# Kernel optimization log

Hardware: AMD Instinct MI355X
Metric: run time of the kernel (lower is better)

Reference implementation:

```python
import jax, jax.numpy as jnp
import numpy as np

# Geometry constants (match init_kwargs)
PHI, T, H, W = 720, 512, 256, 256
ANGLE_RATIO = 1.0
RHO = float(np.sqrt(2.0))          # radius of detector span: ||max_pt-min_pt||/2 for [-1,1]^2
DPHI = float(np.pi) * ANGLE_RATIO / PHI   # uniform angle cell width (== mean angle step)
DT = 2.0 * RHO / T                 # detector cell width
T0 = -RHO + 0.5 * DT               # first detector cell center
DX = 2.0 / H                       # pixel width


def setup_inputs() -> dict:
    key = jax.random.key(0)
    k1, k2 = jax.random.split(key)
    sinos = jax.random.normal(k1, (32, PHI, T), dtype=jnp.float32)
    kernel = jax.random.normal(k2, (T // 2 + 1,), dtype=jnp.float32)
    return {"sinos": sinos, "kernel": kernel}


def _backproject(sino):
    """Parallel-beam backprojection (adjoint Radon), linear interp in t.

    sino: [B, PHI, T] -> image [B, H, W].
    f(x) = sum_phi g(phi, x.cos(phi)+y.sin(phi)) * dphi, zero outside detector.
    """
    angles = (jnp.arange(PHI, dtype=sino.dtype) + 0.5) * DPHI  # cell centers
    xs = (-1.0 + (jnp.arange(H, dtype=sino.dtype) + 0.5) * DX)
    X, Y = jnp.meshgrid(xs, xs, indexing='ij')  # [H, W] pixel centers

    def step(acc, inp):
        g, ang = inp                         # g: [B, T] sinogram slice at angle ang
        t = X * jnp.cos(ang) + Y * jnp.sin(ang)   # [H, W] detector coordinate
        u = (t - T0) / DT                    # fractional detector index
        i0 = jnp.floor(u)
        w = u - i0
        i0 = i0.astype(jnp.int32)
        i1 = i0 + 1
        w0 = jnp.where((i0 >= 0) & (i0 < T), 1.0 - w, 0.0)
        w1 = jnp.where((i1 >= 0) & (i1 < T), w, 0.0)
        i0c = jnp.clip(i0, 0, T - 1)
        i1c = jnp.clip(i1, 0, T - 1)
        v = g[:, i0c] * w0 + g[:, i1c] * w1  # [B, H, W]
        return acc + v, None

    B = sino.shape[0]
    acc0 = jnp.zeros((B, H, W), dtype=sino.dtype)
    sino_p = jnp.moveaxis(sino, 1, 0)        # [PHI, B, T] for scan over angles
    acc, _ = jax.lax.scan(step, acc0, (sino_p, angles))
    return acc * DPHI


def reference(sinos, kernel):
    # FFT-domain 1D filtering along detector axis, then backprojection
    filtered = jnp.fft.irfft(jnp.fft.rfft(sinos, axis=-1) * kernel, n=T, axis=-1)
    return _backproject(filtered.astype(sinos.dtype))
```

## Files before the change

kernel.cpp:

```cpp
#include <hip/hip_runtime.h>
#include <hip/hip_bf16.h>

#define NPHI 720
#define NT   512
#define NH   256
#define NB   32

#define DPHI_F   0.004363323129985824f
#define INV_DT_F 181.01933598375618f
#define DX_F     0.0078125f
#define W2PI_F   0.012271846303085130f

#define FSTR 520

typedef __fp16  h2   __attribute__((ext_vector_type(2)));
typedef _Float16 f16x2 __attribute__((ext_vector_type(2)));
typedef _Float16 f16x8 __attribute__((ext_vector_type(8)));
typedef float    f32x4 __attribute__((ext_vector_type(4)));
typedef float    f32x4u __attribute__((ext_vector_type(4), aligned(4)));
typedef float    f32x2u __attribute__((ext_vector_type(2), aligned(4)));

__device__ __forceinline__ float fdot2f(h2 a, float b_bits, float c) {
    return __builtin_amdgcn_fdot2(__builtin_bit_cast(f16x2, a),
                                  __builtin_bit_cast(f16x2, b_bits), c, false);
}

__global__ __launch_bounds__(256) void setup_kernel(const float* __restrict__ kern,
                                                    float* __restrict__ ws,
                                                    unsigned int* __restrict__ Ht,
                                                    float4* __restrict__ out4,
                                                    float* __restrict__ filt) {
    const int bid = (int)blockIdx.x;
    const int tid = threadIdx.x;
    if (bid < 64) {
        __shared__ float ctab[512];
        __shared__ float kk[257];
        __shared__ float hloc[512];
        kk[tid] = kern[tid];
        if (tid == 0) kk[256] = kern[256];
        ctab[tid]       = cosf((float)tid * W2PI_F);
        ctab[tid + 256] = cosf((float)(tid + 256) * W2PI_F);
        __syncthreads();
        for (int tt = tid; tt < 512; tt += 256) {
            float acc = 0.f;
            for (int k = 1; k < 256; ++k)
                acc += kk[k] * ctab[(k * tt) & 511];
            hloc[tt] = (kk[0] + ((tt & 1) ? -kk[256] : kk[256]) + 2.f * acc) * (1.f / 512.f);
        }
        __syncthreads();
        const int o  = bid * 8 + (tid >> 5);
        const int c0 = tid & 31;
        unsigned int* dst = Ht + (size_t)o * 256;
        #pragma unroll
        for (int k = 0; k < 8; ++k) {
            int mp = c0 + 32 * k;
            h2 p = __builtin_amdgcn_cvt_pkrtz(hloc[(o - 2 * mp) & 511],
                                              hloc[(o - 2 * mp - 1) & 511]);
            dst[mp] = __builtin_bit_cast(unsigned int, p);
        }
    } else if (bid < 67) {
        int p = (bid - 64) * 256 + tid;
        if (p < NPHI) {
            float ang = ((float)p + 0.5f) * DPHI_F;
            float s, c;
            sincosf(ang, &s, &c);
            float cd = c * INV_DT_F;
            float sd = s * INV_DT_F;
            ws[512 + 4 * p + 0] = cd;
            ws[512 + 4 * p + 1] = sd;
            ws[512 + 4 * p + 2] = cd * DX_F;
            ws[512 + 4 * p + 3] = sd * DX_F;
        }
    } else if (bid < 195) {
        const float4 z = make_float4(0.f, 0.f, 0.f, 0.f);
        const int nout4 = NB * NH * NH / 4;
        for (int i = (bid - 67) * 256 + tid; i < nout4; i += 128 * 256)
            out4[i] = z;
    } else {
        const float4 z = make_float4(0.f, 0.f, 0.f, 0.f);
        const int rb = (bid - 195) * 180;
        for (int i = tid; i < 360; i += 256) {
            int row = rb + (i >> 1);
            float* p = filt + (size_t)row * FSTR + ((i & 1) ? 516 : 0);
            *(float4*)p = z;
        }
    }
}

#define ASTR 40
#define BSTR 40

__global__ __launch_bounds__(512) void conv_gemm_kernel(const float* __restrict__ g,
                                                        const unsigned short* __restrict__ Ht,
                                                        float* __restrict__ filt) {
    __shared__ __attribute__((aligned(16))) unsigned short As[64 * ASTR];
    __shared__ __attribute__((aligned(16))) unsigned short Bs[512 * BSTR];
    const int tid = threadIdx.x;
    const int m0 = (int)blockIdx.x * 64;

    const int w = tid >> 6, l = tid & 63;
    const int wm = (w >> 2) * 32;
    const int wn = (w & 3) * 128;
    const int fr = l & 15, g16 = l >> 4;

    const int arow = tid >> 3, aq = (tid & 7) * 4;

    f32x4 acc[2][8];
    #pragma unroll
    for (int i = 0; i < 2; ++i)
        #pragma unroll
        for (int j = 0; j < 8; ++j) acc[i][j] = (f32x4){0.f, 0.f, 0.f, 0.f};

    for (int k0 = 0; k0 < 512; k0 += 32) {
        __syncthreads();
        {
            const float* src = g + (size_t)(m0 + arow) * NT + (k0 + aq);
            float4 v = *(const float4*)src;
            h2 p0 = __builtin_amdgcn_cvt_pkrtz(v.x, v.y);
            h2 p1 = __builtin_amdgcn_cvt_pkrtz(v.z, v.w);
            *(uint2*)&As[arow * ASTR + aq] =
                make_uint2(__builtin_bit_cast(unsigned int, p0),
                           __builtin_bit_cast(unsigned int, p1));
        }
        {
            const float4* src = (const float4*)(Ht + (size_t)tid * NT + k0);
            float4 v0 = src[0], v1 = src[1], v2 = src[2], v3 = src[3];
            unsigned short* dst = &Bs[tid * BSTR];
            *(float4*)(dst)      = v0;
            *(float4*)(dst + 8)  = v1;
            *(float4*)(dst + 16) = v2;
            *(float4*)(dst + 24) = v3;
        }
        __syncthreads();

        f16x8 af[2], bf[8];
        #pragma unroll
        for (int i = 0; i < 2; ++i)
            af[i] = *(const f16x8*)&As[(wm + i * 16 + fr) * ASTR + g16 * 8];
        #pragma unroll
        for (int j = 0; j < 8; ++j)
            bf[j] = *(const f16x8*)&Bs[(wn + j * 16 + fr) * BSTR + g16 * 8];
        #pragma unroll
        for (int i = 0; i < 2; ++i)
            #pragma unroll
            for (int j = 0; j < 8; ++j)
                acc[i][j] = __builtin_amdgcn_mfma_f32_16x16x32_f16(af[i], bf[j], acc[i][j], 0, 0, 0);
    }

    #pragma unroll
    for (int i = 0; i < 2; ++i)
        #pragma unroll
        for (int j = 0; j < 8; ++j)
            #pragma unroll
            for (int v = 0; v < 4; ++v) {
                int row = m0 + wm + i * 16 + g16 * 4 + v;
                int col = wn + j * 16 + fr;
                filt[(size_t)row * FSTR + 4 + col] = acc[i][j][v];
            }
}

#define WCHUNK 15
#define WSTR   82

__global__ __launch_bounds__(256, 8) void backproject_kernel(const float* __restrict__ filt,
                                                             const float* __restrict__ ws,
                                                             float* __restrict__ out) {
    __shared__ __attribute__((aligned(16))) float2 win01[WCHUNK * WSTR];
    __shared__ __attribute__((aligned(16))) float2 win23[WCHUNK * WSTR];
    __shared__ float cstbuf[WCHUNK];

    const int tid  = threadIdx.x;
    const int bidx = (int)blockIdx.x;
    const int quarter = bidx >> 9;
    const int rem  = bidx & 511;
    const int b    = (rem >> 6) * 4;
    const int tile = rem & 63;
    const int i0 = (tile >> 3) * 32;
    const int j0 = (tile & 7) * 32;

    const float* trig = ws + 512;

    const int w  = tid >> 6;
    const int l  = tid & 63;
    const int wi = (w >> 1) * 16, wj = (w & 1) * 16;
    const int li = l >> 3, lj = l & 7;
    const int pi = i0 + wi + 2 * li;
    const int pj = j0 + wj + 2 * lj;
    const float xi = -1.f + ((float)pi + 0.5f) * DX_F;
    const float yj = -1.f + ((float)pj + 0.5f) * DX_F;

    const int sa = tid >> 4;
    const int st = tid & 15;
    const float xlo = -1.f + ((float)i0 + 0.5f) * DX_F;
    const float xhi = xlo + 31.f * DX_F;
    const float ylo = -1.f + ((float)j0 + 0.5f) * DX_F;
    const float yhi = ylo + 31.f * DX_F;

    const float* fb0 = filt + (size_t)b * (NPHI * FSTR);

    float acc[4][2][2];
    #pragma unroll
    for (int bb = 0; bb < 4; ++bb)
        #pragma unroll
        for (int di = 0; di < 2; ++di)
            #pragma unroll
            for (int dj = 0; dj < 2; ++dj) acc[bb][di][dj] = 0.f;

    const int pbeg = quarter * 180;
    for (int p0 = pbeg; p0 < pbeg + 180; p0 += WCHUNK) {
        __syncthreads();
        if (sa < WCHUNK && st < 14) {
            const int p = p0 + sa;
            const float4 tg = *(const float4*)&trig[p * 4];
            const float umin = 256.5f + fminf(xlo * tg.x, xhi * tg.x)
                                      + fminf(ylo * tg.y, yhi * tg.y);
            const float b0f = floorf(umin) - 1.f;
            if (st == 0) cstbuf[sa] = 256.5f - b0f;
            const int b0 = (int)b0f;
            const int base  = b0 + 5 * st - 1;
            const int basec = min(base, 506);
            float f[4][6];
            #pragma unroll
            for (int bb = 0; bb < 4; ++bb) {
                const float* rr = fb0 + (size_t)bb * (NPHI * FSTR) + (size_t)p * FSTR + 4 + basec;
                f32x4u v0 = *(const f32x4u*)rr;
                f32x2u v1 = *(const f32x2u*)(rr + 4);
                f[bb][0] = v0[0]; f[bb][1] = v0[1]; f[bb][2] = v0[2];
                f[bb][3] = v0[3]; f[bb][4] = v1[0]; f[bb][5] = v1[1];
            }
            const int s0 = sa * WSTR + (basec - b0 + 1);
            #pragma unroll
            for (int j = 0; j < 5; ++j) {
                h2 a0 = __builtin_amdgcn_cvt_pkrtz(f[0][j], f[0][j + 1]);
                h2 a1 = __builtin_amdgcn_cvt_pkrtz(f[1][j], f[1][j + 1]);
                h2 a2 = __builtin_amdgcn_cvt_pkrtz(f[2][j], f[2][j + 1]);
                h2 a3 = __builtin_amdgcn_cvt_pkrtz(f[3][j], f[3][j + 1]);
                win01[s0 + j] = make_float2(__builtin_bit_cast(float, a0),
                                            __builtin_bit_cast(float, a1));
                win23[s0 + j] = make_float2(__builtin_bit_cast(float, a2),
                                            __builtin_bit_cast(float, a3));
            }
        }
        __syncthreads();

        #pragma unroll 3
        for (int a = 0; a < WCHUNK; ++a) {
            const float4 tg = *(const float4*)&trig[(p0 + a) * 4];
            const float cst = cstbuf[a];
            const float2* wr01 = &win01[a * WSTR];
            const float2* wr23 = &win23[a * WSTR];
            const float u00 = xi * tg.x + yj * tg.y + cst;
            #pragma unroll
            for (int di = 0; di < 2; ++di) {
                float u = di ? (u00 + tg.z) : u00;
                #pragma unroll
                for (int dj = 0; dj < 2; ++dj) {
                    float fl = floorf(u);
                    float wv = u - fl;
                    int  ip  = (int)fl;
                    h2   wp  = __builtin_amdgcn_cvt_pkrtz(1.f - wv, wv);
                    float2 s01 = wr01[ip];
                    float2 s23 = wr23[ip];
                    acc[0][di][dj] = fdot2f(wp, s01.x, acc[0][di][dj]);
                    acc[1][di][dj] = fdot2f(wp, s01.y, acc[1][di][dj]);
                    acc[2][di][dj] = fdot2f(wp, s23.x, acc[2][di][dj]);
                    acc[3][di][dj] = fdot2f(wp, s23.y, acc[3][di][dj]);
                    u += tg.w;
                }
            }
        }
    }

    #pragma unroll
    for (int bb = 0; bb < 4; ++bb) {
        float* ob = out + (size_t)(b + bb) * (NH * NH) + (size_t)pi * NH + pj;
        #pragma unroll
        for (int di = 0; di < 2; ++di)
            #pragma unroll
            for (int dj = 0; dj < 2; ++dj)
                unsafeAtomicAdd(ob + di * NH + dj, acc[bb][di][dj] * DPHI_F);
    }
}

extern "C" void kernel_launch(void* const* d_in, const int* in_sizes, int n_in,
                              void* d_out, int out_size, void* d_ws, size_t ws_size,
                              hipStream_t stream) {
    const float* sinos = (const float*)d_in[0];
    const float* kern  = (const float*)d_in[1];
    float* out = (float*)d_out;
    float* ws  = (float*)d_ws;

    unsigned int*   Ht32 = (unsigned int*)(ws + 4096);
    unsigned short* Ht   = (unsigned short*)Ht32;
    float*          filt = ws + 4096 + 131072;

    hipLaunchKernelGGL(setup_kernel, dim3(323), dim3(256), 0, stream,
                       kern, ws, Ht32, (float4*)out, filt);
    hipLaunchKernelGGL(conv_gemm_kernel, dim3(23040 / 64), dim3(512), 0, stream,
                       sinos, Ht, filt);
    hipLaunchKernelGGL(backproject_kernel, dim3(4 * (NB / 4) * 64), dim3(256), 0, stream,
                       filt, ws, out);
}
```

Baseline: 207.5 us.

## Fuse filter setup into conv GEMM and batch eight sinograms per backprojection block

The filter kernel setup, the zeroing work and the convolution GEMM now run as one front kernel. Each GEMM block builds the circulant filter matrix in shared memory once and indexes it cyclically, so it no longer reloads the Ht matrix from global memory on every k-step. The backprojection now handles 8 batches per block across 6 angle slices, with a smaller angle chunk and lower occupancy. This reuses each interpolation weight across more batches at the cost of more registers and recomputing the filter in every GEMM block.

```diff
diff --git a/kernel.cpp b/kernel.cpp
--- a/kernel.cpp
+++ b/kernel.cpp
@@ -25,41 +25,105 @@
                                   __builtin_bit_cast(f16x2, b_bits), c, false);
 }
 
-__global__ __launch_bounds__(256) void setup_kernel(const float* __restrict__ kern,
+#define ASTR 40
+#define BSTR 40
+
+__global__ __launch_bounds__(512) void front_kernel(const float* __restrict__ g,
+                                                    const float* __restrict__ kern,
                                                     float* __restrict__ ws,
-                                                    unsigned int* __restrict__ Ht,
                                                     float4* __restrict__ out4,
                                                     float* __restrict__ filt) {
+    __shared__ __attribute__((aligned(16))) unsigned short As[64 * ASTR];
+    __shared__ __attribute__((aligned(16))) unsigned short Bs[512 * BSTR];
+    __shared__ float hloc[512];
     const int bid = (int)blockIdx.x;
     const int tid = threadIdx.x;
-    if (bid < 64) {
-        __shared__ float ctab[512];
-        __shared__ float kk[257];
-        __shared__ float hloc[512];
-        kk[tid] = kern[tid];
-        if (tid == 0) kk[256] = kern[256];
-        ctab[tid]       = cosf((float)tid * W2PI_F);
-        ctab[tid + 256] = cosf((float)(tid + 256) * W2PI_F);
-        __syncthreads();
-        for (int tt = tid; tt < 512; tt += 256) {
+
+    if (bid < 360) {
+        float* ctab = (float*)As;
+        float* kkp  = (float*)Bs;
+        if (tid < 257) kkp[tid] = kern[tid];
+        ctab[tid] = cosf((float)tid * W2PI_F);
+        __syncthreads();
+        {
             float acc = 0.f;
             for (int k = 1; k < 256; ++k)
-                acc += kk[k] * ctab[(k * tt) & 511];
-            hloc[tt] = (kk[0] + ((tt & 1) ? -kk[256] : kk[256]) + 2.f * acc) * (1.f / 512.f);
-        }
-        __syncthreads();
-        const int o  = bid * 8 + (tid >> 5);
-        const int c0 = tid & 31;
-        unsigned int* dst = Ht + (size_t)o * 256;
-        #pragma unroll
-        for (int k = 0; k < 8; ++k) {
-            int mp = c0 + 32 * k;
-            h2 p = __builtin_amdgcn_cvt_pkrtz(hloc[(o - 2 * mp) & 511],
-                                              hloc[(o - 2 * mp - 1) & 511]);
-            dst[mp] = __builtin_bit_cast(unsigned int, p);
-        }
-    } else if (bid < 67) {
-        int p = (bid - 64) * 256 + tid;
+                acc += kkp[k] * ctab[(k * tid) & 511];
+            hloc[tid] = (kkp[0] + ((tid & 1) ? -kkp[256] : kkp[256]) + 2.f * acc)
+                        * (1.f / 512.f);
+        }
+        __syncthreads();
+        {
+            unsigned int uu[16];
+            #pragma unroll
+            for (int q = 0; q < 16; ++q) {
+                float lo = hloc[(tid - 2 * q) & 511];
+                float hi = hloc[(tid - 2 * q - 1) & 511];
+                h2 p = __builtin_amdgcn_cvt_pkrtz(lo, hi);
+                uu[q] = __builtin_bit_cast(unsigned int, p);
+            }
+            unsigned int* dst = (unsigned int*)&Bs[tid * BSTR];
+            *(uint4*)(dst)      = make_uint4(uu[0], uu[1], uu[2], uu[3]);
+            *(uint4*)(dst + 4)  = make_uint4(uu[4], uu[5], uu[6], uu[7]);
+            *(uint4*)(dst + 8)  = make_uint4(uu[8], uu[9], uu[10], uu[11]);
+            *(uint4*)(dst + 12) = make_uint4(uu[12], uu[13], uu[14], uu[15]);
+        }
+
+        const int m0 = bid * 64;
+        const int w = tid >> 6, l = tid & 63;
+        const int wm = (w >> 2) * 32;
+        const int wn = (w & 3) * 128;
+        const int fr = l & 15, g16 = l >> 4;
+        const int arow = tid >> 3, aq = (tid & 7) * 4;
+
+        f32x4 acc[2][8];
+        #pragma unroll
+        for (int i = 0; i < 2; ++i)
+            #pragma unroll
+            for (int j = 0; j < 8; ++j) acc[i][j] = (f32x4){0.f, 0.f, 0.f, 0.f};
+
+        for (int k0 = 0; k0 < 512; k0 += 32) {
+            __syncthreads();
+            {
+                const float* src = g + (size_t)(m0 + arow) * NT + (k0 + aq);
+                float4 v = *(const float4*)src;
+                h2 p0 = __builtin_amdgcn_cvt_pkrtz(v.x, v.y);
+                h2 p1 = __builtin_amdgcn_cvt_pkrtz(v.z, v.w);
+                *(uint2*)&As[arow * ASTR + aq] =
+                    make_uint2(__builtin_bit_cast(unsigned int, p0),
+                               __builtin_bit_cast(unsigned int, p1));
+            }
+            __syncthreads();
+
+            f16x8 af[2], bf[8];
+            #pragma unroll
+            for (int i = 0; i < 2; ++i)
+                af[i] = *(const f16x8*)&As[(wm + i * 16 + fr) * ASTR + g16 * 8];
+            const int rbase = (wn + fr - k0) & 511;
+            #pragma unroll
+            for (int j = 0; j < 8; ++j) {
+                const int row = (rbase + j * 16) & 511;
+                bf[j] = *(const f16x8*)&Bs[row * BSTR + g16 * 8];
+            }
+            #pragma unroll
+            for (int i = 0; i < 2; ++i)
+                #pragma unroll
+                for (int j = 0; j < 8; ++j)
+                    acc[i][j] = __builtin_amdgcn_mfma_f32_16x16x32_f16(af[i], bf[j], acc[i][j], 0, 0, 0);
+        }
+
+        #pragma unroll
+        for (int i = 0; i < 2; ++i)
+            #pragma unroll
+            for (int j = 0; j < 8; ++j)
+                #pragma unroll
+                for (int v = 0; v < 4; ++v) {
+                    int row = m0 + wm + i * 16 + g16 * 4 + v;
+                    int col = wn + j * 16 + fr;
+                    filt[(size_t)row * FSTR + 4 + col] = acc[i][j][v];
+                }
+    } else if (bid < 362) {
+        int p = (bid - 360) * 512 + tid;
         if (p < NPHI) {
             float ang = ((float)p + 0.5f) * DPHI_F;
             float s, c;
@@ -71,109 +135,37 @@
             ws[512 + 4 * p + 2] = cd * DX_F;
             ws[512 + 4 * p + 3] = sd * DX_F;
         }
-    } else if (bid < 195) {
+    } else if (bid < 426) {
         const float4 z = make_float4(0.f, 0.f, 0.f, 0.f);
         const int nout4 = NB * NH * NH / 4;
-        for (int i = (bid - 67) * 256 + tid; i < nout4; i += 128 * 256)
+        for (int i = (bid - 362) * 512 + tid; i < nout4; i += 64 * 512)
             out4[i] = z;
     } else {
         const float4 z = make_float4(0.f, 0.f, 0.f, 0.f);
-        const int rb = (bid - 195) * 180;
-        for (int i = tid; i < 360; i += 256) {
-            int row = rb + (i >> 1);
+        const int nslots = 23040 * 2;
+        for (int i = (bid - 426) * 512 + tid; i < nslots; i += 64 * 512) {
+            int row = i >> 1;
             float* p = filt + (size_t)row * FSTR + ((i & 1) ? 516 : 0);
             *(float4*)p = z;
         }
     }
 }
 
-#define ASTR 40
-#define BSTR 40
-
-__global__ __launch_bounds__(512) void conv_gemm_kernel(const float* __restrict__ g,
-                                                        const unsigned short* __restrict__ Ht,
-                                                        float* __restrict__ filt) {
-    __shared__ __attribute__((aligned(16))) unsigned short As[64 * ASTR];
-    __shared__ __attribute__((aligned(16))) unsigned short Bs[512 * BSTR];
-    const int tid = threadIdx.x;
-    const int m0 = (int)blockIdx.x * 64;
-
-    const int w = tid >> 6, l = tid & 63;
-    const int wm = (w >> 2) * 32;
-    const int wn = (w & 3) * 128;
-    const int fr = l & 15, g16 = l >> 4;
-
-    const int arow = tid >> 3, aq = (tid & 7) * 4;
-
-    f32x4 acc[2][8];
-    #pragma unroll
-    for (int i = 0; i < 2; ++i)
-        #pragma unroll
-        for (int j = 0; j < 8; ++j) acc[i][j] = (f32x4){0.f, 0.f, 0.f, 0.f};
-
-    for (int k0 = 0; k0 < 512; k0 += 32) {
-        __syncthreads();
-        {
-            const float* src = g + (size_t)(m0 + arow) * NT + (k0 + aq);
-            float4 v = *(const float4*)src;
-            h2 p0 = __builtin_amdgcn_cvt_pkrtz(v.x, v.y);
-            h2 p1 = __builtin_amdgcn_cvt_pkrtz(v.z, v.w);
-            *(uint2*)&As[arow * ASTR + aq] =
-                make_uint2(__builtin_bit_cast(unsigned int, p0),
-                           __builtin_bit_cast(unsigned int, p1));
-        }
-        {
-            const float4* src = (const float4*)(Ht + (size_t)tid * NT + k0);
-            float4 v0 = src[0], v1 = src[1], v2 = src[2], v3 = src[3];
-            unsigned short* dst = &Bs[tid * BSTR];
-            *(float4*)(dst)      = v0;
-            *(float4*)(dst + 8)  = v1;
-            *(float4*)(dst + 16) = v2;
-            *(float4*)(dst + 24) = v3;
-        }
-        __syncthreads();
-
-        f16x8 af[2], bf[8];
-        #pragma unroll
-        for (int i = 0; i < 2; ++i)
-            af[i] = *(const f16x8*)&As[(wm + i * 16 + fr) * ASTR + g16 * 8];
-        #pragma unroll
-        for (int j = 0; j < 8; ++j)
-            bf[j] = *(const f16x8*)&Bs[(wn + j * 16 + fr) * BSTR + g16 * 8];
-        #pragma unroll
-        for (int i = 0; i < 2; ++i)
-            #pragma unroll
-            for (int j = 0; j < 8; ++j)
-                acc[i][j] = __builtin_amdgcn_mfma_f32_16x16x32_f16(af[i], bf[j], acc[i][j], 0, 0, 0);
-    }
-
-    #pragma unroll
-    for (int i = 0; i < 2; ++i)
-        #pragma unroll
-        for (int j = 0; j < 8; ++j)
-            #pragma unroll
-            for (int v = 0; v < 4; ++v) {
-                int row = m0 + wm + i * 16 + g16 * 4 + v;
-                int col = wn + j * 16 + fr;
-                filt[(size_t)row * FSTR + 4 + col] = acc[i][j][v];
-            }
-}
-
-#define WCHUNK 15
+#define WCHUNK 10
 #define WSTR   82
-
-__global__ __launch_bounds__(256, 8) void backproject_kernel(const float* __restrict__ filt,
+#define WREG   (WCHUNK * WSTR)
+
+__global__ __launch_bounds__(256, 6) void backproject_kernel(const float* __restrict__ filt,
                                                              const float* __restrict__ ws,
                                                              float* __restrict__ out) {
-    __shared__ __attribute__((aligned(16))) float2 win01[WCHUNK * WSTR];
-    __shared__ __attribute__((aligned(16))) float2 win23[WCHUNK * WSTR];
+    __shared__ __attribute__((aligned(16))) float2 win[4][WREG];
     __shared__ float cstbuf[WCHUNK];
 
     const int tid  = threadIdx.x;
     const int bidx = (int)blockIdx.x;
-    const int quarter = bidx >> 9;
-    const int rem  = bidx & 511;
-    const int b    = (rem >> 6) * 4;
+    const int sixth = bidx >> 8;
+    const int rem  = bidx & 255;
+    const int b    = (rem >> 6) * 8;
     const int tile = rem & 63;
     const int i0 = (tile >> 3) * 32;
     const int j0 = (tile & 7) * 32;
@@ -198,16 +190,16 @@
 
     const float* fb0 = filt + (size_t)b * (NPHI * FSTR);
 
-    float acc[4][2][2];
+    float acc[8][2][2];
     #pragma unroll
-    for (int bb = 0; bb < 4; ++bb)
+    for (int bb = 0; bb < 8; ++bb)
         #pragma unroll
         for (int di = 0; di < 2; ++di)
             #pragma unroll
             for (int dj = 0; dj < 2; ++dj) acc[bb][di][dj] = 0.f;
 
-    const int pbeg = quarter * 180;
-    for (int p0 = pbeg; p0 < pbeg + 180; p0 += WCHUNK) {
+    const int pbeg = sixth * 120;
+    for (int p0 = pbeg; p0 < pbeg + 120; p0 += WCHUNK) {
         __syncthreads();
         if (sa < WCHUNK && st < 14) {
             const int p = p0 + sa;
@@ -219,36 +211,34 @@
             const int b0 = (int)b0f;
             const int base  = b0 + 5 * st - 1;
             const int basec = min(base, 506);
-            float f[4][6];
-            #pragma unroll
-            for (int bb = 0; bb < 4; ++bb) {
-                const float* rr = fb0 + (size_t)bb * (NPHI * FSTR) + (size_t)p * FSTR + 4 + basec;
-                f32x4u v0 = *(const f32x4u*)rr;
-                f32x2u v1 = *(const f32x2u*)(rr + 4);
-                f[bb][0] = v0[0]; f[bb][1] = v0[1]; f[bb][2] = v0[2];
-                f[bb][3] = v0[3]; f[bb][4] = v1[0]; f[bb][5] = v1[1];
-            }
             const int s0 = sa * WSTR + (basec - b0 + 1);
             #pragma unroll
-            for (int j = 0; j < 5; ++j) {
-                h2 a0 = __builtin_amdgcn_cvt_pkrtz(f[0][j], f[0][j + 1]);
-                h2 a1 = __builtin_amdgcn_cvt_pkrtz(f[1][j], f[1][j + 1]);
-                h2 a2 = __builtin_amdgcn_cvt_pkrtz(f[2][j], f[2][j + 1]);
-                h2 a3 = __builtin_amdgcn_cvt_pkrtz(f[3][j], f[3][j + 1]);
-                win01[s0 + j] = make_float2(__builtin_bit_cast(float, a0),
-                                            __builtin_bit_cast(float, a1));
-                win23[s0 + j] = make_float2(__builtin_bit_cast(float, a2),
-                                            __builtin_bit_cast(float, a3));
-            }
-        }
-        __syncthreads();
-
-        #pragma unroll 3
+            for (int pp = 0; pp < 4; ++pp) {
+                const float* rA = fb0 + (size_t)(2 * pp) * (NPHI * FSTR)
+                                      + (size_t)p * FSTR + 4 + basec;
+                const float* rB = rA + (size_t)(NPHI * FSTR);
+                f32x4u a0 = *(const f32x4u*)rA;
+                f32x2u a1 = *(const f32x2u*)(rA + 4);
+                f32x4u c0 = *(const f32x4u*)rB;
+                f32x2u c1 = *(const f32x2u*)(rB + 4);
+                float fA[6] = {a0[0], a0[1], a0[2], a0[3], a1[0], a1[1]};
+                float fB[6] = {c0[0], c0[1], c0[2], c0[3], c1[0], c1[1]};
+                #pragma unroll
+                for (int j = 0; j < 5; ++j) {
+                    h2 pa = __builtin_amdgcn_cvt_pkrtz(fA[j], fA[j + 1]);
+                    h2 pb = __builtin_amdgcn_cvt_pkrtz(fB[j], fB[j + 1]);
+                    win[pp][s0 + j] = make_float2(__builtin_bit_cast(float, pa),
+                                                  __builtin_bit_cast(float, pb));
+                }
+            }
+        }
+        __syncthreads();
+
+        #pragma unroll 2
         for (int a = 0; a < WCHUNK; ++a) {
             const float4 tg = *(const float4*)&trig[(p0 + a) * 4];
             const float cst = cstbuf[a];
-            const float2* wr01 = &win01[a * WSTR];
-            const float2* wr23 = &win23[a * WSTR];
+            const float2* wr = &win[0][a * WSTR];
             const float u00 = xi * tg.x + yj * tg.y + cst;
             #pragma unroll
             for (int di = 0; di < 2; ++di) {
@@ -259,12 +249,18 @@
                     float wv = u - fl;
                     int  ip  = (int)fl;
                     h2   wp  = __builtin_amdgcn_cvt_pkrtz(1.f - wv, wv);
-                    float2 s01 = wr01[ip];
-                    float2 s23 = wr23[ip];
+                    float2 s01 = wr[ip];
+                    float2 s23 = wr[ip + WREG];
+                    float2 s45 = wr[ip + 2 * WREG];
+                    float2 s67 = wr[ip + 3 * WREG];
                     acc[0][di][dj] = fdot2f(wp, s01.x, acc[0][di][dj]);
                     acc[1][di][dj] = fdot2f(wp, s01.y, acc[1][di][dj]);
                     acc[2][di][dj] = fdot2f(wp, s23.x, acc[2][di][dj]);
                     acc[3][di][dj] = fdot2f(wp, s23.y, acc[3][di][dj]);
+                    acc[4][di][dj] = fdot2f(wp, s45.x, acc[4][di][dj]);
+                    acc[5][di][dj] = fdot2f(wp, s45.y, acc[5][di][dj]);
+                    acc[6][di][dj] = fdot2f(wp, s67.x, acc[6][di][dj]);
+                    acc[7][di][dj] = fdot2f(wp, s67.y, acc[7][di][dj]);
                     u += tg.w;
                 }
             }
@@ -272,7 +268,7 @@
     }
 
     #pragma unroll
-    for (int bb = 0; bb < 4; ++bb) {
+    for (int bb = 0; bb < 8; ++bb) {
         float* ob = out + (size_t)(b + bb) * (NH * NH) + (size_t)pi * NH + pj;
         #pragma unroll
         for (int di = 0; di < 2; ++di)
@@ -290,14 +286,10 @@
     float* out = (float*)d_out;
     float* ws  = (float*)d_ws;
 
-    unsigned int*   Ht32 = (unsigned int*)(ws + 4096);
-    unsigned short* Ht   = (unsigned short*)Ht32;
-    float*          filt = ws + 4096 + 131072;
-
-    hipLaunchKernelGGL(setup_kernel, dim3(323), dim3(256), 0, stream,
-                       kern, ws, Ht32, (float4*)out, filt);
-    hipLaunchKernelGGL(conv_gemm_kernel, dim3(23040 / 64), dim3(512), 0, stream,
-                       sinos, Ht, filt);
-    hipLaunchKernelGGL(backproject_kernel, dim3(4 * (NB / 4) * 64), dim3(256), 0, stream,
+    float* filt = ws + 4096;
+
+    hipLaunchKernelGGL(front_kernel, dim3(490), dim3(512), 0, stream,
+                       sinos, kern, ws, (float4*)out, filt);
+    hipLaunchKernelGGL(backproject_kernel, dim3(6 * (NB / 8) * 64), dim3(256), 0, stream,
                        filt, ws, out);
 }
```

New measurement: 198.1 us. 1.05x faster.
